# Optimization experiments

Measured on AMD Instinct MI355X. Metric: run time of the kernel, lower is better.

Reference implementation:

```python
import jax, jax.numpy as jnp
import numpy as np

NUM_HEADS = 16
KEY_DEPTH = 1024


def setup_inputs() -> dict:
    key = jax.random.key(0)
    ks = jax.random.split(key, 7)
    B, L, D = 2, 2048, 1024
    scale = 1.0 / np.sqrt(D)
    return {
        "query_antecedent": jax.random.normal(ks[0], (B, L, D), jnp.float32),
        "memory_antecedent": jax.random.normal(ks[1], (B, L, D), jnp.float32),
        "bias": jax.random.normal(ks[2], (1, 1, L, L), jnp.float32),
        "Wq": jax.random.normal(ks[3], (D, KEY_DEPTH), jnp.float32) * scale,
        "Wk": jax.random.normal(ks[4], (D, KEY_DEPTH), jnp.float32) * scale,
        "Wv": jax.random.normal(ks[5], (D, KEY_DEPTH), jnp.float32) * scale,
        "Wo": jax.random.normal(ks[6], (KEY_DEPTH, D), jnp.float32) * scale,
    }


def _split_heads(x, h):
    # [B, L, D] -> [B, H, L, D/H]
    b, l, d = x.shape
    return x.reshape(b, l, h, d // h).transpose(0, 2, 1, 3)


def reference(query_antecedent, memory_antecedent, bias, Wq, Wk, Wv, Wo):
    h = NUM_HEADS
    d_head = KEY_DEPTH // h
    q = _split_heads(query_antecedent @ Wq, h) * (d_head ** -0.5)
    k = _split_heads(memory_antecedent @ Wk, h)
    v = _split_heads(memory_antecedent @ Wv, h)
    # [B, H, Lq, Lk]
    logits = jnp.einsum("bhqd,bhkd->bhqk", q, k) + bias
    weights = jax.nn.softmax(logits, axis=-1)
    x = jnp.einsum("bhqk,bhkd->bhqd", weights, v)
    # combine heads: [B, H, L, d] -> [B, L, H*d]
    b, _, l, d = x.shape
    x = x.transpose(0, 2, 1, 3).reshape(b, l, h * d)
    return x @ Wo
```

## Files before the change

### kernel.cpp

```cpp
#include <hip/hip_runtime.h>
#include <hip/hip_bf16.h>


typedef __attribute__((ext_vector_type(8))) short short8;
typedef __attribute__((ext_vector_type(4))) short short4v;
typedef __attribute__((ext_vector_type(4))) float float4v;

#define BATCH 2
#define LSEQ 2048
#define DMODEL 1024
#define NHEADS 16
#define DHEAD 64
#define MROWS 4096
#define QKVLD 3072

__global__ __launch_bounds__(256)
void convert_kernel(const float* __restrict__ qa, const float* __restrict__ ma,
                    __hip_bfloat16* __restrict__ qo, __hip_bfloat16* __restrict__ mo)
{
    const size_t i = ((size_t)blockIdx.x * 256 + threadIdx.x) * 8;
    const float* src = blockIdx.y ? ma : qa;
    __hip_bfloat16* dst = blockIdx.y ? mo : qo;
    float4 v0 = *reinterpret_cast<const float4*>(src + i);
    float4 v1 = *reinterpret_cast<const float4*>(src + i + 4);
    union { __hip_bfloat16 h[8]; int4 v; } pk;
    pk.h[0] = (__hip_bfloat16)v0.x; pk.h[1] = (__hip_bfloat16)v0.y;
    pk.h[2] = (__hip_bfloat16)v0.z; pk.h[3] = (__hip_bfloat16)v0.w;
    pk.h[4] = (__hip_bfloat16)v1.x; pk.h[5] = (__hip_bfloat16)v1.y;
    pk.h[6] = (__hip_bfloat16)v1.z; pk.h[7] = (__hip_bfloat16)v1.w;
    *reinterpret_cast<int4*>(dst + i) = pk.v;
}

__global__ __launch_bounds__(256)
void transpose_w_kernel(const float* __restrict__ W0, const float* __restrict__ W1,
                        const float* __restrict__ W2, const float* __restrict__ W3,
                        __hip_bfloat16* __restrict__ T0, __hip_bfloat16* __restrict__ T1,
                        __hip_bfloat16* __restrict__ T2, __hip_bfloat16* __restrict__ T3)
{
    __shared__ __hip_bfloat16 T[64][68];

    const float* W; __hip_bfloat16* D;
    if      (blockIdx.z == 0) { W = W0; D = T0; }
    else if (blockIdx.z == 1) { W = W1; D = T1; }
    else if (blockIdx.z == 2) { W = W2; D = T2; }
    else                      { W = W3; D = T3; }

    const int t  = threadIdx.x;
    const int n0 = blockIdx.x * 64;
    const int k0 = blockIdx.y * 64;

#pragma unroll
    for (int p = 0; p < 4; ++p) {
        const int r = p * 16 + (t >> 4);
        const int c = (t & 15) * 4;
        float4 v = *reinterpret_cast<const float4*>(&W[(size_t)(k0 + r) * DMODEL + n0 + c]);
        union { __hip_bfloat16 h[4]; ushort4 v; } pk;
        pk.h[0] = (__hip_bfloat16)v.x; pk.h[1] = (__hip_bfloat16)v.y;
        pk.h[2] = (__hip_bfloat16)v.z; pk.h[3] = (__hip_bfloat16)v.w;
        *reinterpret_cast<ushort4*>(&T[r][c]) = pk.v;
    }
    __syncthreads();
#pragma unroll
    for (int p = 0; p < 2; ++p) {
        const int n  = p * 32 + (t & 31);
        const int kc = (t >> 5) * 8;
        union { __hip_bfloat16 h[8]; int4 v; } pk;
#pragma unroll
        for (int j = 0; j < 8; ++j) pk.h[j] = T[kc + j][n];
        *reinterpret_cast<int4*>(&D[(size_t)(n0 + n) * DMODEL + k0 + kc]) = pk.v;
    }
}

#define GBK 64

template<int BMT>
__global__ __launch_bounds__(256, 2)
void gemm_bt_kernel(const __hip_bfloat16* __restrict__ A0,
                    const __hip_bfloat16* __restrict__ A1, int nsplit,
                    float alpha0, float alpha1,
                    const __hip_bfloat16* __restrict__ Bt,
                    float* __restrict__ Cf, __hip_bfloat16* __restrict__ Cb,
                    int K, int ldc, int nbx)
{
    __shared__ __hip_bfloat16 As[BMT][GBK];
    __shared__ __hip_bfloat16 Bs[128][GBK];

    const int t    = threadIdx.x;
    const int w    = t >> 6;
    const int lane = t & 63;
    const int l15  = lane & 15;
    const int lq   = lane >> 4;
    const int wm   = (w >> 1) * (BMT / 2);
    const int wn   = (w & 1) * 64;
    const int MI   = BMT / 32;

    const int nwg  = gridDim.x;
    const int c    = blockIdx.x & 7;
    const int q    = blockIdx.x >> 3;
    const int mper = (nwg >> 3) / nbx;
    const int m0   = (c * mper + q / nbx) * BMT;
    const int n0   = (q % nbx) * 128;

    const __hip_bfloat16* A = (n0 < nsplit) ? A0 : A1;
    const float alpha = (n0 < nsplit) ? alpha0 : alpha1;

    const int lrow = lane >> 3;
    const int lch  = (lane & 7) ^ lrow;

    float4v acc[BMT / 32][4];
#pragma unroll
    for (int mi = 0; mi < MI; ++mi)
#pragma unroll
        for (int ni = 0; ni < 4; ++ni) acc[mi][ni] = (float4v){0.f, 0.f, 0.f, 0.f};

    for (int k0 = 0; k0 < K; k0 += GBK) {
        __syncthreads();
#pragma unroll
        for (int i = 0; i < BMT / 32; ++i) {
            const int rb = (w * (BMT / 32) + i) * 8;
            const int r  = rb + lrow;
            __builtin_amdgcn_global_load_lds(
                (const __attribute__((address_space(1))) void*)
                    (A + (size_t)(m0 + r) * K + k0 + lch * 8),
                (__attribute__((address_space(3))) void*)&As[rb][0], 16, 0, 0);
        }
#pragma unroll
        for (int i = 0; i < 4; ++i) {
            const int rb = (w * 4 + i) * 8;
            const int r  = rb + lrow;
            __builtin_amdgcn_global_load_lds(
                (const __attribute__((address_space(1))) void*)
                    (Bt + (size_t)(n0 + r) * K + k0 + lch * 8),
                (__attribute__((address_space(3))) void*)&Bs[rb][0], 16, 0, 0);
        }
        asm volatile("s_waitcnt vmcnt(0)" ::: "memory");
        __syncthreads();

#pragma unroll
        for (int kh = 0; kh < 2; ++kh) {
            short8 af[BMT / 32], bf[4];
#pragma unroll
            for (int mi = 0; mi < MI; ++mi) {
                const int r = wm + mi * 16 + l15;
                af[mi] = *reinterpret_cast<const short8*>(
                    &As[r][(((kh << 2) | lq) ^ (r & 7)) << 3]);
            }
#pragma unroll
            for (int ni = 0; ni < 4; ++ni) {
                const int r = wn + ni * 16 + l15;
                bf[ni] = *reinterpret_cast<const short8*>(
                    &Bs[r][(((kh << 2) | lq) ^ (r & 7)) << 3]);
            }
#pragma unroll
            for (int mi = 0; mi < MI; ++mi)
#pragma unroll
                for (int ni = 0; ni < 4; ++ni)
                    acc[mi][ni] = __builtin_amdgcn_mfma_f32_16x16x32_bf16(
                        af[mi], bf[ni], acc[mi][ni], 0, 0, 0);
        }
    }

#pragma unroll
    for (int mi = 0; mi < MI; ++mi)
#pragma unroll
        for (int ni = 0; ni < 4; ++ni)
#pragma unroll
            for (int r = 0; r < 4; ++r) {
                const int row = m0 + wm + mi * 16 + lq * 4 + r;
                const int col = n0 + wn + ni * 16 + l15;
                const float v = acc[mi][ni][r] * alpha;
                if (Cf) Cf[(size_t)row * ldc + col] = v;
                else    Cb[(size_t)row * ldc + col] = (__hip_bfloat16)v;
            }
}

#define KSTR 68
#define PSTR 132

__global__ __launch_bounds__(512, 2)
void attn_mfma_kernel(const __hip_bfloat16* __restrict__ QKV,
                      const float* __restrict__ bias,
                      __hip_bfloat16* __restrict__ X)
{
    __shared__ __hip_bfloat16 Ks[128][KSTR];
    __shared__ __hip_bfloat16 Vt[64][PSTR];

    const int t   = threadIdx.x;
    const int w   = t >> 6;
    const int l15 = t & 15;
    const int lq  = (t & 63) >> 4;

    const int bid = blockIdx.x;
    const int r8  = bid & 7;
    const int j   = bid >> 3;
    const int bh  = r8 + 8 * (j >> 3);
    const int q0  = (j & 7) * 256;
    const int b   = bh >> 4;
    const int h   = bh & 15;

    const __hip_bfloat16* Kb = QKV + (size_t)b * LSEQ * QKVLD + 1024 + h * DHEAD;
    const __hip_bfloat16* Vb = Kb + 1024;

    short8 aq[2][2];
#pragma unroll
    for (int g = 0; g < 2; ++g) {
        const __hip_bfloat16* qrow = QKV +
            (size_t)(b * LSEQ + q0 + w * 32 + g * 16 + l15) * QKVLD + h * DHEAD + lq * 8;
        aq[g][0] = *reinterpret_cast<const short8*>(qrow);
        aq[g][1] = *reinterpret_cast<const short8*>(qrow + 32);
    }

    const float* bp0 = bias + (size_t)(q0 + w * 32 + l15) * LSEQ + lq * 4;
    const float* bp1 = bp0 + (size_t)16 * LSEQ;

    float lsum[2] = {0.f, 0.f};
    float4v o_acc[2][4];
#pragma unroll
    for (int g = 0; g < 2; ++g)
#pragma unroll
        for (int n = 0; n < 4; ++n) o_acc[g][n] = (float4v){0.f, 0.f, 0.f, 0.f};

    const int skey = t >> 2;
    const int sdh  = (t & 3) * 16;
    const int a    = t & 3;
    const int cblk = ((skey >> 5) << 2) | ((skey >> 2) & 3);
    const int vcol = (((cblk ^ (a << 2)) << 3)) | ((((skey >> 4) & 1) << 2)) | (skey & 3);

    int4 pk0, pk1, pv0, pv1;
    {
        const __hip_bfloat16* ks = Kb + (size_t)skey * QKVLD + sdh;
        pk0 = *reinterpret_cast<const int4*>(ks);
        pk1 = *reinterpret_cast<const int4*>(ks + 8);
        const __hip_bfloat16* vs = Vb + (size_t)skey * QKVLD + sdh;
        pv0 = *reinterpret_cast<const int4*>(vs);
        pv1 = *reinterpret_cast<const int4*>(vs + 8);
    }

    for (int kt = 0; kt < LSEQ / 128; ++kt) {
        const int k0 = kt * 128;
        __syncthreads();
        *reinterpret_cast<int4*>(&Ks[skey][sdh])     = pk0;
        *reinterpret_cast<int4*>(&Ks[skey][sdh + 8]) = pk1;
        {
            const __hip_bfloat16* vp0 = reinterpret_cast<const __hip_bfloat16*>(&pv0);
            const __hip_bfloat16* vp1 = reinterpret_cast<const __hip_bfloat16*>(&pv1);
#pragma unroll
            for (int jj = 0; jj < 8; ++jj) Vt[sdh + jj][vcol]     = vp0[jj];
#pragma unroll
            for (int jj = 0; jj < 8; ++jj) Vt[sdh + 8 + jj][vcol] = vp1[jj];
        }
        {
            const int knext = (kt + 1 < LSEQ / 128) ? k0 + 128 : k0;
            const __hip_bfloat16* ks = Kb + (size_t)(knext + skey) * QKVLD + sdh;
            pk0 = *reinterpret_cast<const int4*>(ks);
            pk1 = *reinterpret_cast<const int4*>(ks + 8);
            const __hip_bfloat16* vs = Vb + (size_t)(knext + skey) * QKVLD + sdh;
            pv0 = *reinterpret_cast<const int4*>(vs);
            pv1 = *reinterpret_cast<const int4*>(vs + 8);
        }
        __syncthreads();

#pragma unroll
        for (int m = 0; m < 4; ++m) {
            short8 bkA0 = *reinterpret_cast<const short8*>(&Ks[(2*m)    *16 + l15][lq * 8]);
            short8 bkA1 = *reinterpret_cast<const short8*>(&Ks[(2*m)    *16 + l15][32 + lq * 8]);
            short8 bkB0 = *reinterpret_cast<const short8*>(&Ks[(2*m + 1)*16 + l15][lq * 8]);
            short8 bkB1 = *reinterpret_cast<const short8*>(&Ks[(2*m + 1)*16 + l15][32 + lq * 8]);

            float4v sA[2], sB[2];
#pragma unroll
            for (int g = 0; g < 2; ++g) {
                sA[g] = (float4v){0.f, 0.f, 0.f, 0.f};
                sB[g] = (float4v){0.f, 0.f, 0.f, 0.f};
            }
            __builtin_amdgcn_s_setprio(1);
#pragma unroll
            for (int g = 0; g < 2; ++g) {
                sA[g] = __builtin_amdgcn_mfma_f32_16x16x32_bf16(bkA0, aq[g][0], sA[g], 0, 0, 0);
                sA[g] = __builtin_amdgcn_mfma_f32_16x16x32_bf16(bkA1, aq[g][1], sA[g], 0, 0, 0);
                sB[g] = __builtin_amdgcn_mfma_f32_16x16x32_bf16(bkB0, aq[g][0], sB[g], 0, 0, 0);
                sB[g] = __builtin_amdgcn_mfma_f32_16x16x32_bf16(bkB1, aq[g][1], sB[g], 0, 0, 0);
            }
            __builtin_amdgcn_s_setprio(0);

            short8 pf[2];
#pragma unroll
            for (int g = 0; g < 2; ++g) {
                const float* bp = g ? bp1 : bp0;
                float4v bvA = *reinterpret_cast<const float4v*>(bp + k0 + 32 * m);
                float4v bvB = *reinterpret_cast<const float4v*>(bp + k0 + 32 * m + 16);
                union { __hip_bfloat16 hh[8]; short8 v; } pp;
#pragma unroll
                for (int r = 0; r < 4; ++r) {
                    const float e = __expf(sA[g][r] + bvA[r]);
                    lsum[g] += e;
                    pp.hh[r] = (__hip_bfloat16)e;
                }
#pragma unroll
                for (int r = 0; r < 4; ++r) {
                    const float e = __expf(sB[g][r] + bvB[r]);
                    lsum[g] += e;
                    pp.hh[4 + r] = (__hip_bfloat16)e;
                }
                pf[g] = pp.v;
            }

            short8 vt[4];
#pragma unroll
            for (int n = 0; n < 4; ++n)
                vt[n] = *reinterpret_cast<const short8*>(
                    &Vt[n * 16 + l15][((m * 4 + lq) ^ (n << 2)) << 3]);

            __builtin_amdgcn_s_setprio(1);
#pragma unroll
            for (int g = 0; g < 2; ++g)
#pragma unroll
                for (int n = 0; n < 4; ++n)
                    o_acc[g][n] = __builtin_amdgcn_mfma_f32_16x16x32_bf16(
                        vt[n], pf[g], o_acc[g][n], 0, 0, 0);
            __builtin_amdgcn_s_setprio(0);
        }
    }

#pragma unroll
    for (int g = 0; g < 2; ++g) {
        lsum[g] += __shfl_xor(lsum[g], 16);
        lsum[g] += __shfl_xor(lsum[g], 32);
        const float inv = 1.f / lsum[g];
        const int row = q0 + w * 32 + g * 16 + l15;
        __hip_bfloat16* dst = X + (size_t)(b * LSEQ + row) * DMODEL + h * DHEAD + lq * 4;
#pragma unroll
        for (int n = 0; n < 4; ++n) {
            union { __hip_bfloat16 hh[4]; short4v v; } o;
#pragma unroll
            for (int r = 0; r < 4; ++r) o.hh[r] = (__hip_bfloat16)(o_acc[g][n][r] * inv);
            *reinterpret_cast<short4v*>(dst + n * 16) = o.v;
        }
    }
}

extern "C" void kernel_launch(void* const* d_in, const int* in_sizes, int n_in,
                              void* d_out, int out_size, void* d_ws, size_t ws_size,
                              hipStream_t stream)
{
    const float* qa   = (const float*)d_in[0];
    const float* ma   = (const float*)d_in[1];
    const float* bias = (const float*)d_in[2];
    const float* Wq   = (const float*)d_in[3];
    const float* Wk   = (const float*)d_in[4];
    const float* Wv   = (const float*)d_in[5];
    const float* Wo   = (const float*)d_in[6];
    float* out = (float*)d_out;

    char* wsb = (char*)d_ws;
    __hip_bfloat16* qa16 = (__hip_bfloat16*)(wsb);
    __hip_bfloat16* ma16 = (__hip_bfloat16*)(wsb + (8u << 20));
    __hip_bfloat16* Wt   = (__hip_bfloat16*)(wsb + (16u << 20));
    __hip_bfloat16* Wot  = (__hip_bfloat16*)(wsb + (22u << 20));
    __hip_bfloat16* QKVw = (__hip_bfloat16*)(wsb + (24u << 20));
    __hip_bfloat16* Xw   = qa16;

    convert_kernel<<<dim3(MROWS * DMODEL / (256 * 8), 2), 256, 0, stream>>>(
        qa, ma, qa16, ma16);

    transpose_w_kernel<<<dim3(16, 16, 4), 256, 0, stream>>>(
        Wq, Wk, Wv, Wo,
        Wt, Wt + (size_t)DMODEL * DMODEL, Wt + 2 * (size_t)DMODEL * DMODEL, Wot);

    gemm_bt_kernel<128><<<dim3(768), 256, 0, stream>>>(
        qa16, ma16, DMODEL, 0.125f, 1.0f, Wt, nullptr, QKVw, DMODEL, QKVLD, 24);

    attn_mfma_kernel<<<dim3(256), 512, 0, stream>>>(QKVw, bias, Xw);

    gemm_bt_kernel<64><<<dim3(512), 256, 0, stream>>>(
        Xw, Xw, DMODEL + 1, 1.0f, 1.0f, Wot, out, nullptr, DMODEL, DMODEL, 8);
}
```

Before: 249.4 us.

## Split attention key chunks across warp halves and double block count

Each attention block now covers 128 query rows instead of 256, and the launch grows to 512 blocks. Within a block, warps 0-3 and 4-7 take different halves of every 128-key tile. The two partial outputs and row sums are combined through shared memory, reusing the K/V buffers, before normalisation and the store. The launch bound is raised to 4 blocks per CU to add occupancy. The cost is an extra reduction pass, two more barriers and more register pressure.

```diff
diff --git a/kernel.cpp b/kernel.cpp
--- a/kernel.cpp
+++ b/kernel.cpp
@@ -177,24 +177,28 @@
 #define KSTR 68
 #define PSTR 132
 
-__global__ __launch_bounds__(512, 2)
+__global__ __launch_bounds__(512, 4)
 void attn_mfma_kernel(const __hip_bfloat16* __restrict__ QKV,
                       const float* __restrict__ bias,
                       __hip_bfloat16* __restrict__ X)
 {
-    __shared__ __hip_bfloat16 Ks[128][KSTR];
-    __shared__ __hip_bfloat16 Vt[64][PSTR];
+    __shared__ __align__(16) char smem[34816];
+    auto Ks = reinterpret_cast<__hip_bfloat16(*)[KSTR]>(smem);
+    auto Vt = reinterpret_cast<__hip_bfloat16(*)[PSTR]>(smem + 17408);
+    auto Of = reinterpret_cast<float(*)[68]>(smem);
 
     const int t   = threadIdx.x;
     const int w   = t >> 6;
+    const int r   = w & 3;
+    const int kk  = w >> 2;
     const int l15 = t & 15;
     const int lq  = (t & 63) >> 4;
 
     const int bid = blockIdx.x;
     const int r8  = bid & 7;
     const int j   = bid >> 3;
-    const int bh  = r8 + 8 * (j >> 3);
-    const int q0  = (j & 7) * 256;
+    const int bh  = r8 + 8 * (j >> 4);
+    const int q0  = (j & 15) * 128;
     const int b   = bh >> 4;
     const int h   = bh & 15;
 
@@ -205,12 +209,12 @@
 #pragma unroll
     for (int g = 0; g < 2; ++g) {
         const __hip_bfloat16* qrow = QKV +
-            (size_t)(b * LSEQ + q0 + w * 32 + g * 16 + l15) * QKVLD + h * DHEAD + lq * 8;
+            (size_t)(b * LSEQ + q0 + r * 32 + g * 16 + l15) * QKVLD + h * DHEAD + lq * 8;
         aq[g][0] = *reinterpret_cast<const short8*>(qrow);
         aq[g][1] = *reinterpret_cast<const short8*>(qrow + 32);
     }
 
-    const float* bp0 = bias + (size_t)(q0 + w * 32 + l15) * LSEQ + lq * 4;
+    const float* bp0 = bias + (size_t)(q0 + r * 32 + l15) * LSEQ + lq * 4;
     const float* bp1 = bp0 + (size_t)16 * LSEQ;
 
     float lsum[2] = {0.f, 0.f};
@@ -261,7 +265,8 @@
         __syncthreads();
 
 #pragma unroll
-        for (int m = 0; m < 4; ++m) {
+        for (int mm = 0; mm < 2; ++mm) {
+            const int m = kk * 2 + mm;
             short8 bkA0 = *reinterpret_cast<const short8*>(&Ks[(2*m)    *16 + l15][lq * 8]);
             short8 bkA1 = *reinterpret_cast<const short8*>(&Ks[(2*m)    *16 + l15][32 + lq * 8]);
             short8 bkB0 = *reinterpret_cast<const short8*>(&Ks[(2*m + 1)*16 + l15][lq * 8]);
@@ -291,16 +296,16 @@
                 float4v bvB = *reinterpret_cast<const float4v*>(bp + k0 + 32 * m + 16);
                 union { __hip_bfloat16 hh[8]; short8 v; } pp;
 #pragma unroll
-                for (int r = 0; r < 4; ++r) {
-                    const float e = __expf(sA[g][r] + bvA[r]);
-                    lsum[g] += e;
-                    pp.hh[r] = (__hip_bfloat16)e;
+                for (int e = 0; e < 4; ++e) {
+                    const float ev = __expf(sA[g][e] + bvA[e]);
+                    lsum[g] += ev;
+                    pp.hh[e] = (__hip_bfloat16)ev;
                 }
 #pragma unroll
-                for (int r = 0; r < 4; ++r) {
-                    const float e = __expf(sB[g][r] + bvB[r]);
-                    lsum[g] += e;
-                    pp.hh[4 + r] = (__hip_bfloat16)e;
+                for (int e = 0; e < 4; ++e) {
+                    const float ev = __expf(sB[g][e] + bvB[e]);
+                    lsum[g] += ev;
+                    pp.hh[4 + e] = (__hip_bfloat16)ev;
                 }
                 pf[g] = pp.v;
             }
@@ -326,15 +331,38 @@
     for (int g = 0; g < 2; ++g) {
         lsum[g] += __shfl_xor(lsum[g], 16);
         lsum[g] += __shfl_xor(lsum[g], 32);
-        const float inv = 1.f / lsum[g];
-        const int row = q0 + w * 32 + g * 16 + l15;
-        __hip_bfloat16* dst = X + (size_t)(b * LSEQ + row) * DMODEL + h * DHEAD + lq * 4;
-#pragma unroll
-        for (int n = 0; n < 4; ++n) {
-            union { __hip_bfloat16 hh[4]; short4v v; } o;
-#pragma unroll
-            for (int r = 0; r < 4; ++r) o.hh[r] = (__hip_bfloat16)(o_acc[g][n][r] * inv);
-            *reinterpret_cast<short4v*>(dst + n * 16) = o.v;
+    }
+
+    __syncthreads();
+    if (kk == 1) {
+#pragma unroll
+        for (int g = 0; g < 2; ++g) {
+            const int row = r * 32 + g * 16 + l15;
+#pragma unroll
+            for (int n = 0; n < 4; ++n)
+                *reinterpret_cast<float4v*>(&Of[row][n * 16 + lq * 4]) = o_acc[g][n];
+            if (lq == 0) Of[row][64] = lsum[g];
+        }
+    }
+    __syncthreads();
+    if (kk == 0) {
+#pragma unroll
+        for (int g = 0; g < 2; ++g) {
+            const int row = r * 32 + g * 16 + l15;
+#pragma unroll
+            for (int n = 0; n < 4; ++n)
+                o_acc[g][n] += *reinterpret_cast<const float4v*>(&Of[row][n * 16 + lq * 4]);
+            const float inv = 1.f / (lsum[g] + Of[row][64]);
+            __hip_bfloat16* dst =
+                X + (size_t)(b * LSEQ + q0 + row) * DMODEL + h * DHEAD + lq * 4;
+#pragma unroll
+            for (int n = 0; n < 4; ++n) {
+                union { __hip_bfloat16 hh[4]; short4v v; } o;
+#pragma unroll
+                for (int e = 0; e < 4; ++e)
+                    o.hh[e] = (__hip_bfloat16)(o_acc[g][n][e] * inv);
+                *reinterpret_cast<short4v*>(dst + n * 16) = o.v;
+            }
         }
     }
 }
@@ -370,7 +398,7 @@
     gemm_bt_kernel<128><<<dim3(768), 256, 0, stream>>>(
         qa16, ma16, DMODEL, 0.125f, 1.0f, Wt, nullptr, QKVw, DMODEL, QKVLD, 24);
 
-    attn_mfma_kernel<<<dim3(256), 512, 0, stream>>>(QKVw, bias, Xw);
+    attn_mfma_kernel<<<dim3(512), 512, 0, stream>>>(QKVw, bias, Xw);
 
     gemm_bt_kernel<64><<<dim3(512), 256, 0, stream>>>(
         Xw, Xw, DMODEL + 1, 1.0f, 1.0f, Wot, out, nullptr, DMODEL, DMODEL, 8);
```

Measured after the change: 306.6 us. +22.9%, slower.
